# Kernel optimization log

Measured on AMD Instinct MI355X. Metric: run time of the kernel, lower is better.

The kernel has to match this reference:

```python
import jax, jax.numpy as jnp
import numpy as np

BS, T, NN, NF = 4, 64, 128, 16
HID, HEADS, RH, LD = 64, 4, 256, 64
EPG = 1024  # edges per graph


def _gat(x, src, dst, N, W, a_s, a_d, b, heads, out_dim, concat):
    # x: [N, Fin] -> h: [N, H, F]
    h = (x @ W).reshape(N, heads, out_dim)
    al_s = jnp.sum(h * a_s[None], axis=-1)  # [N, H]
    al_d = jnp.sum(h * a_d[None], axis=-1)
    e = jax.nn.leaky_relu(al_s[src] + al_d[dst], 0.2)  # [E, H]
    m = jax.ops.segment_max(e, dst, num_segments=N)
    m = jnp.where(jnp.isfinite(m), m, 0.0)
    ex = jnp.exp(e - m[dst])
    den = jax.ops.segment_sum(ex, dst, num_segments=N)
    alpha = ex / (den[dst] + 1e-16)
    agg = jax.ops.segment_sum(h[src] * alpha[:, :, None], dst, num_segments=N)
    o = agg.reshape(N, heads * out_dim) if concat else agg.mean(axis=1)
    return o + b


def _lstm(xs, Wih, Whh, bih, bhh, H):
    # xs: [T, B, D]; PyTorch gate order i,f,g,o
    B = xs.shape[1]
    h0 = jnp.zeros((B, H), xs.dtype)
    c0 = jnp.zeros((B, H), xs.dtype)

    def step(carry, xt):
        h, c = carry
        g = xt @ Wih.T + h @ Whh.T + bih + bhh
        i, f, gg, o = jnp.split(g, 4, axis=-1)
        c = jax.nn.sigmoid(f) * c + jax.nn.sigmoid(i) * jnp.tanh(gg)
        h = jax.nn.sigmoid(o) * jnp.tanh(c)
        return (h, c), None

    (hT, _), _ = jax.lax.scan(step, (h0, c0), xs)
    return hT


def setup_inputs() -> dict:
    key = jax.random.key(0)
    ks = jax.random.split(key, 32)
    s = 0.1
    d = {
        'x': jax.random.normal(ks[0], (BS, T, NN, NF), jnp.float32),
        'edge_index': jax.random.randint(ks[1], (2, EPG), 0, NN),
        'gat0_W': s * jax.random.normal(ks[2], (NF, HEADS * HID)),
        'gat0_asrc': s * jax.random.normal(ks[3], (HEADS, HID)),
        'gat0_adst': s * jax.random.normal(ks[4], (HEADS, HID)),
        'gat0_b': jnp.zeros((HEADS * HID,)),
        'gat1_W': s * jax.random.normal(ks[5], (HEADS * HID, HEADS * HID)),
        'gat1_asrc': s * jax.random.normal(ks[6], (HEADS, HID)),
        'gat1_adst': s * jax.random.normal(ks[7], (HEADS, HID)),
        'gat1_b': jnp.zeros((HEADS * HID,)),
        'gat2_W': s * jax.random.normal(ks[8], (HEADS * HID, HID)),
        'gat2_asrc': s * jax.random.normal(ks[9], (1, HID)),
        'gat2_adst': s * jax.random.normal(ks[10], (1, HID)),
        'gat2_b': jnp.zeros((HID,)),
        'Wih_f': s * jax.random.normal(ks[11], (4 * RH, HID)),
        'Whh_f': s * jax.random.normal(ks[12], (4 * RH, RH)),
        'bih_f': jnp.zeros((4 * RH,)),
        'bhh_f': jnp.zeros((4 * RH,)),
        'Wih_b': s * jax.random.normal(ks[13], (4 * RH, HID)),
        'Whh_b': s * jax.random.normal(ks[14], (4 * RH, RH)),
        'bih_b': jnp.zeros((4 * RH,)),
        'bhh_b': jnp.zeros((4 * RH,)),
        'mu_W': s * jax.random.normal(ks[15], (LD, 2 * RH)),
        'mu_b': jnp.zeros((LD,)),
        'lv_W': s * jax.random.normal(ks[16], (LD, 2 * RH)),
        'lv_b': jnp.zeros((LD,)),
    }
    return d


def reference(x, edge_index, gat0_W, gat0_asrc, gat0_adst, gat0_b,
              gat1_W, gat1_asrc, gat1_adst, gat1_b,
              gat2_W, gat2_asrc, gat2_adst, gat2_b,
              Wih_f, Whh_f, bih_f, bhh_f, Wih_b, Whh_b, bih_b, bhh_b,
              mu_W, mu_b, lv_W, lv_b):
    bs, t, nn, nf = x.shape
    ng = bs * t
    N = ng * nn
    xt = x.reshape(N, nf)
    # batch the edge index: repeat per graph with node offset, then add self-loops
    off = (jnp.arange(ng) * nn).repeat(edge_index.shape[1])  # [ng*E]
    bsrc = jnp.tile(edge_index[0], ng) + off
    bdst = jnp.tile(edge_index[1], ng) + off
    loops = jnp.arange(N)
    src = jnp.concatenate([bsrc, loops])
    dst = jnp.concatenate([bdst, loops])

    xt = jax.nn.relu(_gat(xt, src, dst, N, gat0_W, gat0_asrc, gat0_adst, gat0_b, HEADS, HID, True))
    xt = jax.nn.relu(_gat(xt, src, dst, N, gat1_W, gat1_asrc, gat1_adst, gat1_b, HEADS, HID, True))
    xt = jax.nn.relu(_gat(xt, src, dst, N, gat2_W, gat2_asrc, gat2_adst, gat2_b, 1, HID, False))

    batch_idx = jnp.arange(ng).repeat(nn)
    graph_embs = jax.ops.segment_sum(xt, batch_idx, num_segments=ng).reshape(bs, t, HID)

    seq = jnp.transpose(graph_embs, (1, 0, 2))  # [T, B, HID]
    h_fwd = _lstm(seq, Wih_f, Whh_f, bih_f, bhh_f, RH)
    h_bwd = _lstm(seq[::-1], Wih_b, Whh_b, bih_b, bhh_b, RH)
    feat = jnp.concatenate([h_fwd, h_bwd], axis=1)  # [B, 2*RH]

    mu = feat @ mu_W.T + mu_b
    logvar = feat @ lv_W.T + lv_b
    # PoincareBall(c=1).projx, float32 eps = 4e-3
    maxnorm = 1.0 - 4e-3
    nrm = jnp.linalg.norm(mu, axis=-1, keepdims=True)
    mu = jnp.where(nrm > maxnorm, mu / nrm * maxnorm, mu)
    return (mu, logvar)
```

## Files before the change

kernel.cpp:

```cpp
#include <hip/hip_runtime.h>
#include <hip/hip_bf16.h>

#define BSZ 4
#define TT 64
#define NNODE 128
#define NFEAT 16
#define HIDD 64
#define NHEAD 4
#define RHID 256
#define LDIM 64
#define EPG 1024
#define NGRAPH (BSZ*TT)
#define NTOT (NGRAPH*NNODE)
#define ESLOTS (EPG+NNODE)

#define WOFF_G0W 0
#define WOFF_G0AS 4096
#define WOFF_G0AD 4352
#define WOFF_G0B 4608
#define WOFF_G1W 4864
#define WOFF_G1AS 70400
#define WOFF_G1AD 70656
#define WOFF_G1B 70912
#define WOFF_G2W 71168
#define WOFF_G2AS 87552
#define WOFF_G2AD 87616
#define WOFF_G2B 87680
#define WOFF_WIHF 87744
#define WOFF_WHHF 153280
#define WOFF_BIHF 415424
#define WOFF_BHHF 416448
#define WOFF_WIHB 417472
#define WOFF_WHHB 483008
#define WOFF_BIHB 745152
#define WOFF_BHHB 746176
#define WOFF_MUW 747200
#define WOFF_MUB 779968
#define WOFF_LVW 780032
#define WOFF_LVB 812800
#define WTOTAL   812864

#define FOFF_WBUF 4096
#define FOFF_CSR  1052672
#define FOFF_SYNC 1314816
#define FOFF_WE   1576960
#define FOFF_BBF  1900000
#define FOFF_XFP  2756608
#define FOFF_XBP  3018752
#define FOFF_HT   3280896
#define FOFF_XSEQ 3282944
#define FOFF_PA   3291136
#define FOFF_PB   5388288
#define FOFF_P    7485440

#define BOFF_G0 0
#define BOFF_G1 4096
#define BOFF_G2 69632
#define BOFF_WF 86016
#define BOFF_WB 151552
#define BTOTAL  217088

#define SP_CVTX  (WTOTAL + BTOTAL)
#define SP_WHH   (SP_CVTX + NTOT*NFEAT)
#define SP_HX    (SP_WHH + 262144)
#define SP_TOTAL (SP_HX + 12288)

#define SENT 0xFFFFFFFFu

typedef __attribute__((ext_vector_type(8))) short short8;
typedef __attribute__((ext_vector_type(4))) float float4v;

__device__ __forceinline__ float b2f(unsigned short u){
  union { unsigned int i; float f; } v; v.i = ((unsigned int)u) << 16; return v.f;
}
__device__ __forceinline__ unsigned short f2b(float f){
  __hip_bfloat16 h = __float2bfloat16(f);
  union { __hip_bfloat16 h; unsigned short u; } v; v.h = h; return v.u;
}
__device__ __forceinline__ float ldf(const void* p, int i, int flag){
  return flag ? b2f(((const unsigned short*)p)[i]) : ((const float*)p)[i];
}
__device__ __forceinline__ float h2f(unsigned short s){
  union { _Float16 hh; unsigned short s; } u; u.s = s; return (float)u.hh;
}
__device__ __forceinline__ unsigned short f2h(float f){
  union { _Float16 hh; unsigned short s; } u; u.hh = (_Float16)f; return u.s;
}
__device__ __forceinline__ int sniff32(const unsigned short* w){
  int ok = 0;
  #pragma unroll
  for (int i = 0; i < 32; ++i){
    float a = fabsf(b2f(w[2 * i]));
    if (a > 1e-8f && a < 4.f) ok++;
  }
  return ok >= 16 ? 1 : 0;
}

struct CvtArgs {
  const void* src[24];
  int off[25];
};
__global__ void setup_kernel(CvtArgs a,
                             float* __restrict__ W, unsigned short* __restrict__ BBF,
                             unsigned short* __restrict__ P, unsigned int* __restrict__ WT,
                             unsigned int* __restrict__ HX,
                             const void* __restrict__ x, const int* __restrict__ ei,
                             int* __restrict__ csr_row, unsigned short* __restrict__ csr_src)
{
  __shared__ int cnt[NNODE];
  __shared__ int off[NNODE];
  __shared__ int wo[NNODE];
  const int tid = threadIdx.x;

  if (blockIdx.x == gridDim.x - 1){
    if (tid < NNODE) cnt[tid] = 0;
    __syncthreads();
    for (int i = tid; i < ESLOTS; i += 256){
      int d = (i < EPG) ? ei[EPG + i] : (i - EPG);
      atomicAdd(&cnt[d], 1);
    }
    __syncthreads();
    if (tid < NNODE) off[tid] = cnt[tid];
    for (int o = 1; o < NNODE; o <<= 1){
      __syncthreads();
      int t = (tid < NNODE && tid >= o) ? off[tid - o] : 0;
      __syncthreads();
      if (tid < NNODE) off[tid] += t;
    }
    __syncthreads();
    if (tid < NNODE){
      wo[tid] = off[tid] - cnt[tid];
      csr_row[tid + 1] = off[tid];
    }
    if (tid == 0) csr_row[0] = 0;
    __syncthreads();
    for (int i = tid; i < ESLOTS; i += 256){
      int s, d;
      if (i < EPG){ s = ei[i]; d = ei[EPG + i]; } else { s = i - EPG; d = i - EPG; }
      int pos = atomicAdd(&wo[d], 1);
      csr_src[pos] = (unsigned short)s;
    }
    return;
  }

  int id = blockIdx.x * blockDim.x + tid;
  if (id >= SP_TOTAL) return;
  int fl = sniff32((const unsigned short*)a.src[0]);
  if (id < WTOTAL){
    int k = 0;
    while (id >= a.off[k + 1]) ++k;
    W[id] = ldf(a.src[k], id - a.off[k], fl);
  } else if (id < WTOTAL + BTOTAL){
    int r = id - WTOTAL;
    float v;
    if (r < BOFF_G1){
      int o = r >> 4, k = r & 15;
      v = ldf(a.src[0], k * 256 + o, fl);
    } else if (r < BOFF_G2){
      int rr = r - BOFF_G1; int o = rr >> 8, k = rr & 255;
      v = ldf(a.src[4], k * 256 + o, fl);
    } else if (r < BOFF_WF){
      int rr = r - BOFF_G2; int o = rr >> 8, k = rr & 255;
      v = ldf(a.src[8], k * 64 + o, fl);
    } else if (r < BOFF_WB){
      int q = r - BOFF_WF; int k = q >> 10, n = q & 1023;
      v = ldf(a.src[12], n * 64 + k, fl);
    } else {
      int q = r - BOFF_WB; int k = q >> 10, n = q & 1023;
      v = ldf(a.src[16], n * 64 + k, fl);
    }
    BBF[r] = f2b(v);
  } else if (id < SP_CVTX + NTOT * NFEAT){
    int r = id - SP_CVTX;
    P[r] = fl ? ((const unsigned short*)x)[r] : f2b(((const float*)x)[r]);
  } else if (id < SP_HX){
    int r0 = id - SP_WHH;
    int c = r0 & 3;
    int lane = (r0 >> 2) & 63;
    int nt = (r0 >> 8) & 15;
    int kc = (r0 >> 12) & 7;
    int m = (r0 >> 15) & 3;
    int dir = r0 >> 17;
    int l = nt * 16 + (lane & 15);
    int u = (l >> 6) * 256 + 64 * m + (l & 63);
    int k0 = kc * 32 + ((lane >> 4) << 3) + 2 * c;
    const void* Wsrc = dir ? a.src[17] : a.src[13];
    unsigned short va = f2b(ldf(Wsrc, u * RHID + k0, fl));
    unsigned short vb = f2b(ldf(Wsrc, u * RHID + k0 + 1, fl));
    WT[r0] = (unsigned int)va | ((unsigned int)vb << 16);
  } else {
    HX[id - SP_HX] = SENT;
  }
}

template<int KV>
__global__ __launch_bounds__(256)
void glayer_kernel(const unsigned short* __restrict__ Pin,
                   const unsigned short* __restrict__ BT,
                   const float* __restrict__ Wbuf,
                   int asoff, int adoff, int boff,
                   const int* __restrict__ csr_row, const unsigned short* __restrict__ csr_src,
                   unsigned short* __restrict__ Pout)
{
  __shared__ unsigned short HT_[128 * 136];
  __shared__ unsigned short AD[128 * 136];
  __shared__ unsigned short ALS16[256];
  __shared__ unsigned short ALD16[256];
  __shared__ int   rowL[132];
  __shared__ unsigned char srcL[1152];

  const int tid = threadIdx.x;
  const int g = blockIdx.x >> 1, hb = blockIdx.x & 1;
  const int c0 = hb * 128;
  const int w = tid >> 6, lane = tid & 63, q = lane >> 4, r = lane & 15;
  unsigned short* Bst = AD;

  for (int i = tid; i < 129; i += 256) rowL[i] = csr_row[i];
  for (int i = tid; i < 1152; i += 256) srcL[i] = (unsigned char)csr_src[i];
  __syncthreads();

  {
    float4v acc0[8], acc1[8];
    #pragma unroll
    for (int i = 0; i < 8; ++i){ acc0[i] = (float4v){0,0,0,0}; acc1[i] = (float4v){0,0,0,0}; }
    const int KR = (KV + 31) / 32;
    for (int kr = 0; kr < KR; ++kr){
      const int kc = kr * 32;
      __syncthreads();
      {
        int n = tid >> 1, kb = (tid & 1) * 16;
        uint4 z = {0,0,0,0}; uint4 v0 = z, v1 = z;
        if (kb < KV)     v0 = *(const uint4*)(BT + (size_t)(c0 + n) * KV + kc + kb);
        if (kb + 8 < KV) v1 = *(const uint4*)(BT + (size_t)(c0 + n) * KV + kc + kb + 8);
        *(uint4*)&Bst[n * 40 + kb] = v0;
        *(uint4*)&Bst[n * 40 + kb + 8] = v1;
      }
      short8 a0 = {0,0,0,0,0,0,0,0}, a1 = {0,0,0,0,0,0,0,0};
      if (KV >= 32 || q < 2){
        a0 = *(const short8*)(Pin + (size_t)(g * 128 + 16 * w       + r) * KV + kc + q * 8);
        a1 = *(const short8*)(Pin + (size_t)(g * 128 + 16 * (w + 4) + r) * KV + kc + q * 8);
      }
      __syncthreads();
      #pragma unroll
      for (int nt = 0; nt < 8; ++nt){
        short8 bf = *(const short8*)&Bst[(16 * nt + r) * 40 + q * 8];
        acc0[nt] = __builtin_amdgcn_mfma_f32_16x16x32_bf16(a0, bf, acc0[nt], 0, 0, 0);
        acc1[nt] = __builtin_amdgcn_mfma_f32_16x16x32_bf16(a1, bf, acc1[nt], 0, 0, 0);
      }
    }
    __syncthreads();
    #pragma unroll
    for (int nt = 0; nt < 8; ++nt)
      #pragma unroll
      for (int i = 0; i < 4; ++i){
        HT_[(16 * nt + r) * 136 + 16 * w       + q * 4 + i] = f2b(acc0[nt][i]);
        HT_[(16 * nt + r) * 136 + 16 * (w + 4) + q * 4 + i] = f2b(acc1[nt][i]);
      }
    __syncthreads();
  }

  {
    float as0 = Wbuf[asoff + c0 + 2 * lane], as1 = Wbuf[asoff + c0 + 2 * lane + 1];
    float ad0 = Wbuf[adoff + c0 + 2 * lane], ad1 = Wbuf[adoff + c0 + 2 * lane + 1];
    for (int it = 0; it < 32; ++it){
      int n = it * 4 + w;
      float e0 = b2f(HT_[(2 * lane) * 136 + n]);
      float e1 = b2f(HT_[(2 * lane + 1) * 136 + n]);
      float vs = e0 * as0 + e1 * as1;
      float vd = e0 * ad0 + e1 * ad1;
      #pragma unroll
      for (int m = 16; m >= 1; m >>= 1){ vs += __shfl_xor(vs, m); vd += __shfl_xor(vd, m); }
      if ((lane & 31) == 0){
        ALS16[n * 2 + (lane >> 5)] = f2h(vs);
        ALD16[n * 2 + (lane >> 5)] = f2h(vd);
      }
    }
  }
  __syncthreads();

  for (int hl = 0; hl < 2; ++hl){
    for (int i = tid; i < 8704; i += 256) ((unsigned int*)AD)[i] = 0;
    __syncthreads();
    if (tid < 128){
      int n = tid;
      float aldv = h2f(ALD16[n * 2 + hl]);
      int rs = rowL[n], re = rowL[n + 1];
      float mx = -3e38f, den = 0.f;
      for (int j = rs; j < re; ++j){
        float v = h2f(ALS16[srcL[j] * 2 + hl]) + aldv;
        v = v > 0.f ? v : 0.2f * v;
        if (v > mx){ den = den * __expf(mx - v) + 1.f; mx = v; }
        else den += __expf(v - mx);
      }
      float iden = 1.f / (den + 1e-16f);
      for (int j = rs; j < re; ++j){
        float v = h2f(ALS16[srcL[j] * 2 + hl]) + aldv;
        v = v > 0.f ? v : 0.2f * v;
        float al = __expf(v - mx) * iden;
        int s = srcL[j];
        AD[n * 136 + s] = f2b(b2f(AD[n * 136 + s]) + al);
      }
    }
    __syncthreads();
    float4v am[2][4];
    #pragma unroll
    for (int mt = 0; mt < 2; ++mt)
      #pragma unroll
      for (int nt = 0; nt < 4; ++nt) am[mt][nt] = (float4v){0,0,0,0};
    #pragma unroll
    for (int kc = 0; kc < 4; ++kc){
      short8 af0 = *(const short8*)&AD[(w * 32      + r) * 136 + kc * 32 + q * 8];
      short8 af1 = *(const short8*)&AD[(w * 32 + 16 + r) * 136 + kc * 32 + q * 8];
      #pragma unroll
      for (int nt = 0; nt < 4; ++nt){
        short8 bf = *(const short8*)&HT_[(hl * 64 + nt * 16 + r) * 136 + kc * 32 + q * 8];
        am[0][nt] = __builtin_amdgcn_mfma_f32_16x16x32_bf16(af0, bf, am[0][nt], 0, 0, 0);
        am[1][nt] = __builtin_amdgcn_mfma_f32_16x16x32_bf16(af1, bf, am[1][nt], 0, 0, 0);
      }
    }
    #pragma unroll
    for (int mt = 0; mt < 2; ++mt)
      #pragma unroll
      for (int nt = 0; nt < 4; ++nt){
        int col = hl * 64 + nt * 16 + r;
        float bz = Wbuf[boff + c0 + col];
        #pragma unroll
        for (int i = 0; i < 4; ++i){
          int dst = w * 32 + mt * 16 + q * 4 + i;
          float v = am[mt][nt][i] + bz;
          v = v > 0.f ? v : 0.f;
          Pout[(size_t)(g * 128 + dst) * 256 + c0 + col] = f2b(v);
        }
      }
    __syncthreads();
  }
}

__global__ __launch_bounds__(256)
void glayer2_kernel(const unsigned short* __restrict__ Pin,
                    const unsigned short* __restrict__ BT,
                    const float* __restrict__ Wbuf,
                    const int* __restrict__ csr_row, const unsigned short* __restrict__ csr_src,
                    unsigned short* __restrict__ XSEQ)
{
  __shared__ unsigned short HT_[64 * 136];
  __shared__ unsigned short AD[128 * 136];
  __shared__ float ALSf[128];
  __shared__ float ALDf[128];
  __shared__ int   rowL[132];
  __shared__ unsigned char srcL[1152];
  __shared__ float pools[4][64];

  const int tid = threadIdx.x;
  const int g = blockIdx.x >> 1, hb = blockIdx.x & 1;
  const int w = tid >> 6, lane = tid & 63, q = lane >> 4, r = lane & 15;
  unsigned short* Bst = AD;

  for (int i = tid; i < 129; i += 256) rowL[i] = csr_row[i];
  for (int i = tid; i < 1152; i += 256) srcL[i] = (unsigned char)csr_src[i];
  __syncthreads();

  {
    float4v acc0[4], acc1[4];
    #pragma unroll
    for (int i = 0; i < 4; ++i){ acc0[i] = (float4v){0,0,0,0}; acc1[i] = (float4v){0,0,0,0}; }
    for (int kr = 0; kr < 8; ++kr){
      const int kc = kr * 32;
      __syncthreads();
      {
        int n = tid >> 2, kb = (tid & 3) * 8;
        uint4 v = *(const uint4*)(BT + (size_t)n * 256 + kc + kb);
        *(uint4*)&Bst[n * 40 + kb] = v;
      }
      short8 a0 = *(const short8*)(Pin + (size_t)(g * 128 + 16 * w       + r) * 256 + kc + q * 8);
      short8 a1 = *(const short8*)(Pin + (size_t)(g * 128 + 16 * (w + 4) + r) * 256 + kc + q * 8);
      __syncthreads();
      #pragma unroll
      for (int nt = 0; nt < 4; ++nt){
        short8 bf = *(const short8*)&Bst[(16 * nt + r) * 40 + q * 8];
        acc0[nt] = __builtin_amdgcn_mfma_f32_16x16x32_bf16(a0, bf, acc0[nt], 0, 0, 0);
        acc1[nt] = __builtin_amdgcn_mfma_f32_16x16x32_bf16(a1, bf, acc1[nt], 0, 0, 0);
      }
    }
    __syncthreads();
    #pragma unroll
    for (int nt = 0; nt < 4; ++nt)
      #pragma unroll
      for (int i = 0; i < 4; ++i){
        HT_[(16 * nt + r) * 136 + 16 * w       + q * 4 + i] = f2b(acc0[nt][i]);
        HT_[(16 * nt + r) * 136 + 16 * (w + 4) + q * 4 + i] = f2b(acc1[nt][i]);
      }
    __syncthreads();
  }

  {
    float asv = Wbuf[WOFF_G2AS + lane];
    float adv = Wbuf[WOFF_G2AD + lane];
    for (int it = 0; it < 32; ++it){
      int n = it * 4 + w;
      float e0 = b2f(HT_[lane * 136 + n]);
      float vs = e0 * asv, vd = e0 * adv;
      #pragma unroll
      for (int m = 32; m >= 1; m >>= 1){ vs += __shfl_xor(vs, m); vd += __shfl_xor(vd, m); }
      if (lane == 0){ ALSf[n] = vs; ALDf[n] = vd; }
    }
  }
  __syncthreads();
  for (int i = tid; i < 8704; i += 256) ((unsigned int*)AD)[i] = 0;
  __syncthreads();
  if (tid < 128){
    int n = tid;
    float aldv = ALDf[n];
    int rs = rowL[n], re = rowL[n + 1];
    float mx = -3e38f, den = 0.f;
    for (int j = rs; j < re; ++j){
      float v = ALSf[srcL[j]] + aldv;
      v = v > 0.f ? v : 0.2f * v;
      if (v > mx){ den = den * __expf(mx - v) + 1.f; mx = v; }
      else den += __expf(v - mx);
    }
    float iden = 1.f / (den + 1e-16f);
    for (int j = rs; j < re; ++j){
      float v = ALSf[srcL[j]] + aldv;
      v = v > 0.f ? v : 0.2f * v;
      float al = __expf(v - mx) * iden;
      int s = srcL[j];
      AD[n * 136 + s] = f2b(b2f(AD[n * 136 + s]) + al);
    }
  }
  __syncthreads();
  float4v am[2][4];
  #pragma unroll
  for (int mt = 0; mt < 2; ++mt)
    #pragma unroll
    for (int nt = 0; nt < 4; ++nt) am[mt][nt] = (float4v){0,0,0,0};
  #pragma unroll
  for (int kc = 0; kc < 4; ++kc){
    short8 af0 = *(const short8*)&AD[(w * 32      + r) * 136 + kc * 32 + q * 8];
    short8 af1 = *(const short8*)&AD[(w * 32 + 16 + r) * 136 + kc * 32 + q * 8];
    #pragma unroll
    for (int nt = 0; nt < 4; ++nt){
      short8 bf = *(const short8*)&HT_[(nt * 16 + r) * 136 + kc * 32 + q * 8];
      am[0][nt] = __builtin_amdgcn_mfma_f32_16x16x32_bf16(af0, bf, am[0][nt], 0, 0, 0);
      am[1][nt] = __builtin_amdgcn_mfma_f32_16x16x32_bf16(af1, bf, am[1][nt], 0, 0, 0);
    }
  }
  float psum[4] = {0.f, 0.f, 0.f, 0.f};
  #pragma unroll
  for (int nt = 0; nt < 4; ++nt){
    int col = nt * 16 + r;
    float bz = Wbuf[WOFF_G2B + col];
    #pragma unroll
    for (int mt = 0; mt < 2; ++mt)
      #pragma unroll
      for (int i = 0; i < 4; ++i){
        float v = am[mt][nt][i] + bz;
        psum[nt] += (v > 0.f ? v : 0.f);
      }
    psum[nt] += __shfl_xor(psum[nt], 16);
    psum[nt] += __shfl_xor(psum[nt], 32);
  }
  if (q == 0){
    #pragma unroll
    for (int nt = 0; nt < 4; ++nt) pools[w][nt * 16 + r] = psum[nt];
  }
  __syncthreads();
  if (tid < 64 && (tid >> 5) == hb){
    float s = pools[0][tid] + pools[1][tid] + pools[2][tid] + pools[3][tid];
    int b = g >> 6, tq = g & 63;
    XSEQ[(size_t)(tq * BSZ + b) * HIDD + tid] = f2b(s);
  }
}

__global__ __launch_bounds__(256)
void mmx2_kernel(const unsigned short* __restrict__ A,
                 const unsigned short* __restrict__ B0, const unsigned short* __restrict__ B1,
                 float* __restrict__ C0, float* __restrict__ C1, int M, int Nc, int K)
{
  __shared__ unsigned short As[64][40];
  __shared__ unsigned short Bs[64][40];
  const unsigned short* Bb = blockIdx.z ? B1 : B0;
  float* C = blockIdx.z ? C1 : C0;
  const int tid = threadIdx.x;
  const int w = tid >> 6, lane = tid & 63, q = lane >> 4, r = lane & 15;
  const int m0 = blockIdx.x * 64, n0 = blockIdx.y * 64;
  float4v acc0 = {0,0,0,0}, acc1 = {0,0,0,0}, acc2 = {0,0,0,0}, acc3 = {0,0,0,0};
  const int arow = tid >> 2, akb = (tid & 3) * 8;
  const int bk = tid >> 3, bnb = (tid & 7) * 8;
  for (int kc = 0; kc < K; kc += 32){
    int kw = K - kc; if (kw > 32) kw = 32;
    if (akb < kw){
      uint4 v = *(const uint4*)(A + (size_t)(m0 + arow) * K + kc + akb);
      *(uint4*)&As[arow][akb] = v;
    } else {
      uint4 z = {0,0,0,0}; *(uint4*)&As[arow][akb] = z;
    }
    if (bk < kw){
      uint4 v = *(const uint4*)(Bb + (size_t)(kc + bk) * Nc + n0 + bnb);
      const unsigned short* vs = (const unsigned short*)&v;
      #pragma unroll
      for (int e = 0; e < 8; ++e) Bs[bnb + e][bk] = vs[e];
    } else {
      #pragma unroll
      for (int e = 0; e < 8; ++e) Bs[bnb + e][bk] = 0;
    }
    __syncthreads();
    short8 af = *(const short8*)&As[16 * w + r][q * 8];
    short8 b0 = *(const short8*)&Bs[r][q * 8];
    short8 b1 = *(const short8*)&Bs[16 + r][q * 8];
    short8 b2 = *(const short8*)&Bs[32 + r][q * 8];
    short8 b3 = *(const short8*)&Bs[48 + r][q * 8];
    acc0 = __builtin_amdgcn_mfma_f32_16x16x32_bf16(af, b0, acc0, 0, 0, 0);
    acc1 = __builtin_amdgcn_mfma_f32_16x16x32_bf16(af, b1, acc1, 0, 0, 0);
    acc2 = __builtin_amdgcn_mfma_f32_16x16x32_bf16(af, b2, acc2, 0, 0, 0);
    acc3 = __builtin_amdgcn_mfma_f32_16x16x32_bf16(af, b3, acc3, 0, 0, 0);
    __syncthreads();
  }
  const int row = m0 + 16 * w + q * 4, col0 = n0 + r;
  #pragma unroll
  for (int i = 0; i < 4; ++i){
    size_t base = (size_t)(row + i) * Nc;
    C[base + col0]      = acc0[i];
    C[base + col0 + 16] = acc1[i];
    C[base + col0 + 32] = acc2[i];
    C[base + col0 + 48] = acc3[i];
  }
}

__global__ __launch_bounds__(256)
void lstm13_kernel(const float* __restrict__ XF, const float* __restrict__ XB,
                   const unsigned int* __restrict__ WT,
                   const float* __restrict__ bih_f, const float* __restrict__ bhh_f,
                   const float* __restrict__ bih_b, const float* __restrict__ bhh_b,
                   unsigned int* __restrict__ HX,
                   float* __restrict__ HT)
{
  __shared__ unsigned int WL[32768];
  __shared__ unsigned int H16[16 * 132];
  __shared__ float glds[4][256];

  const int tid = threadIdx.x;
  const int m = blockIdx.x & 3, dir = blockIdx.x >> 2;
  const int w = tid >> 6, lane = tid & 63, quad = lane >> 4, r = lane & 15;
  const float* Xp = dir ? XB : XF;
  const int ub = tid >> 6, uj = tid & 63;
  unsigned int* HXd = HX + dir * 6144;

  const float* bi = dir ? bih_b : bih_f;
  const float* bh = dir ? bhh_b : bhh_f;
  float bias0 = bi[0 * 256 + 64 * m + uj] + bh[0 * 256 + 64 * m + uj];
  float bias1 = bi[1 * 256 + 64 * m + uj] + bh[1 * 256 + 64 * m + uj];
  float bias2 = bi[2 * 256 + 64 * m + uj] + bh[2 * 256 + 64 * m + uj];
  float bias3 = bi[3 * 256 + 64 * m + uj] + bh[3 * 256 + 64 * m + uj];

  {
    const uint4* WT4 = (const uint4*)(WT + dir * 131072 + m * 32768);
    uint4* WL4 = (uint4*)WL;
    #pragma unroll
    for (int s = 0; s < 32; ++s)
      WL4[s * 256 + tid] = WT4[s * 256 + tid];
  }
  for (int i = tid; i < 16 * 132; i += 256) H16[i] = 0;
  float c = 0.f;
  __syncthreads();

  const uint4* WL4 = (const uint4*)WL;
  const uint4* H16u4 = (const uint4*)H16;

  float4v acc[4];
  auto kchunk = [&](int kc){
    uint4 av = H16u4[(lane & 15) * 33 + kc * 4 + quad];
    short8 af = *(const short8*)&av;
    #pragma unroll
    for (int t = 0; t < 4; ++t){
      int nt = w * 4 + t;
      uint4 bv = WL4[(kc * 16 + nt) * 64 + lane];
      short8 bf = *(const short8*)&bv;
      acc[t] = __builtin_amdgcn_mfma_f32_16x16x32_bf16(af, bf, acc[t], 0, 0, 0);
    }
  };

  for (int t = 0; t < TT; ++t){
    const int tb = dir ? (TT - 1 - t) : t;
    const float* xr = Xp + (size_t)(tb * 4 + ub) * 1024 + 64 * m + uj;
    float x0 = xr[0], x1 = xr[256], x2 = xr[512], x3 = xr[768];

    #pragma unroll
    for (int i = 0; i < 4; ++i) acc[i] = (float4v){0,0,0,0};
    kchunk(2 * m); kchunk(2 * m + 1);
    if (t > 0 && w > 0){
      int qp = (m + w) & 3;
      unsigned int* S = HXd + ((t - 1) % 3) * 2048 + m * 512;
      int b2 = lane >> 5, p2 = lane & 31;
      int i1G = b2 * 128 + 32 * qp + p2;
      int i2G = (b2 + 2) * 128 + 32 * qp + p2;
      int i1L = b2 * 132 + 32 * qp + p2;
      int i2L = (b2 + 2) * 132 + 32 * qp + p2;
      unsigned int v1, v2;
      int guard = 0;
      while ((v1 = __hip_atomic_load(&S[i1G], __ATOMIC_RELAXED, __HIP_MEMORY_SCOPE_AGENT)) == SENT
             && guard < 200000){ __builtin_amdgcn_s_sleep(1); ++guard; }
      guard = 0;
      while ((v2 = __hip_atomic_load(&S[i2G], __ATOMIC_RELAXED, __HIP_MEMORY_SCOPE_AGENT)) == SENT
             && guard < 200000){ __builtin_amdgcn_s_sleep(1); ++guard; }
      H16[i1L] = v1; H16[i2L] = v2;
      __hip_atomic_store(&S[i1G], SENT, __ATOMIC_RELAXED, __HIP_MEMORY_SCOPE_AGENT);
      __hip_atomic_store(&S[i2G], SENT, __ATOMIC_RELAXED, __HIP_MEMORY_SCOPE_AGENT);
    }
    __syncthreads();
    #pragma unroll
    for (int i = 1; i < 4; ++i){
      int qp = (m + i) & 3;
      kchunk(2 * qp); kchunk(2 * qp + 1);
    }
    if (quad == 0){
      #pragma unroll
      for (int tt = 0; tt < 4; ++tt){
        int l = (w * 4 + tt) * 16 + r;
        glds[0][l] = acc[tt][0];
        glds[1][l] = acc[tt][1];
        glds[2][l] = acc[tt][2];
        glds[3][l] = acc[tt][3];
      }
    }
    __syncthreads();

    float gi = glds[ub][uj]        + bias0 + x0;
    float gf = glds[ub][64 + uj]   + bias1 + x1;
    float gg = glds[ub][128 + uj]  + bias2 + x2;
    float go = glds[ub][192 + uj]  + bias3 + x3;
    float si = 1.f / (1.f + __expf(-gi));
    float sf = 1.f / (1.f + __expf(-gf));
    float so = 1.f / (1.f + __expf(-go));
    float tg = 1.f - 2.f / (1.f + __expf(2.f * gg));
    c = sf * c + si * tg;
    float ch = 1.f - 2.f / (1.f + __expf(2.f * c));
    float hval = so * ch;
    if (t == TT - 1){
      HT[(size_t)(dir * 4 + ub) * RHID + (64 * m + uj)] = hval;
      break;
    }
    unsigned int own = f2b(hval);
    unsigned int partner = ((unsigned int)__shfl_xor((int)own, 1)) & 0xffffu;
    unsigned int* S = HXd + (t % 3) * 2048;
    if ((uj & 1) == 0){
      unsigned int v = own | (partner << 16);
      int p = uj >> 1;
      int idxG = ub * 128 + 32 * m + p;
      int idxL = ub * 132 + 32 * m + p;
      H16[idxL] = v;
      #pragma unroll
      for (int cns = 1; cns < 4; ++cns)
        __hip_atomic_store(&S[((m + cns) & 3) * 512 + idxG], v,
                           __ATOMIC_RELAXED, __HIP_MEMORY_SCOPE_AGENT);
    }
    __syncthreads();
  }
}

__global__ __launch_bounds__(512)
void head2_kernel(const float* __restrict__ HT,
                  const float* __restrict__ muW, const float* __restrict__ mub,
                  const float* __restrict__ lvW, const float* __restrict__ lvb,
                  float* __restrict__ out)
{
  __shared__ float feat[4][512];
  __shared__ float muv[4][64];
  __shared__ float lvv[4][64];
  int tid = threadIdx.x;
  for (int i = tid; i < 2048; i += 512){
    int rr = i >> 8, k = i & 255;
    int b = rr & 3, d = rr >> 2;
    feat[b][d * 256 + k] = HT[i];
  }
  __syncthreads();
  int w = tid >> 6, lane = tid & 63;
  for (int job = w; job < 512; job += 8){
    int j = job & 63, b = (job >> 6) & 3, mat = job >> 8;
    const float* W = (mat ? lvW : muW) + (size_t)j * 512;
    float s = 0.f;
    #pragma unroll
    for (int e = 0; e < 8; ++e) s += W[lane * 8 + e] * feat[b][lane * 8 + e];
    #pragma unroll
    for (int mm = 32; mm >= 1; mm >>= 1) s += __shfl_xor(s, mm);
    if (lane == 0){
      float v = s + (mat ? lvb[j] : mub[j]);
      if (mat) lvv[b][j] = v; else muv[b][j] = v;
    }
  }
  __syncthreads();
  if (tid < 256){
    int b = tid >> 6, j = tid & 63;
    float mu = muv[b][j];
    float sq = mu * mu;
    #pragma unroll
    for (int mm = 32; mm >= 1; mm >>= 1) sq += __shfl_xor(sq, mm);
    float nrm = sqrtf(sq);
    const float mxn = 1.0f - 4e-3f;
    if (nrm > mxn) mu = mu / nrm * mxn;
    out[b * 64 + j] = mu;
    out[256 + b * 64 + j] = lvv[b][j];
  }
}

extern "C" void kernel_launch(void* const* d_in, const int* in_sizes, int n_in,
                              void* d_out, int out_size, void* d_ws, size_t ws_size,
                              hipStream_t stream)
{
  const int* ei = (const int*)d_in[1];

  float* FW   = (float*)d_ws;
  float* Wbuf = FW + FOFF_WBUF;
  int*   csr_row = (int*)(FW + FOFF_CSR);
  unsigned short* csr_src = (unsigned short*)(FW + FOFF_CSR + 132);
  float* XFp  = FW + FOFF_XFP;
  float* XBp  = FW + FOFF_XBP;
  float* HT   = FW + FOFF_HT;
  unsigned short* XSEQ = (unsigned short*)(FW + FOFF_XSEQ);
  unsigned short* PA   = (unsigned short*)(FW + FOFF_PA);
  unsigned short* PB   = (unsigned short*)(FW + FOFF_PB);
  unsigned short* Pb   = (unsigned short*)(FW + FOFF_P);
  unsigned int*   WT   = (unsigned int*)(FW + FOFF_WE);
  unsigned short* BBF  = (unsigned short*)(FW + FOFF_BBF);
  unsigned int*   HX   = (unsigned int*)(FW + FOFF_SYNC);

  CvtArgs ca;
  static const int wsz[24] = {4096,256,256,256, 65536,256,256,256, 16384,64,64,64,
                              65536,262144,1024,1024, 65536,262144,1024,1024,
                              32768,64,32768,64};
  {
    int acc = 0;
    for (int k = 0; k < 24; ++k){ ca.src[k] = d_in[2 + k]; ca.off[k] = acc; acc += wsz[k]; }
    ca.off[24] = acc;
  }
  int nblk = (SP_TOTAL + 255) / 256 + 1;
  setup_kernel<<<nblk, 256, 0, stream>>>(ca, Wbuf, BBF, Pb, WT, HX,
                                         d_in[0], ei, csr_row, csr_src);

  glayer_kernel<16><<<512, 256, 0, stream>>>(Pb, BBF + BOFF_G0, Wbuf,
                                             WOFF_G0AS, WOFF_G0AD, WOFF_G0B,
                                             csr_row, csr_src, PA);
  glayer_kernel<256><<<512, 256, 0, stream>>>(PA, BBF + BOFF_G1, Wbuf,
                                              WOFF_G1AS, WOFF_G1AD, WOFF_G1B,
                                              csr_row, csr_src, PB);
  glayer2_kernel<<<512, 256, 0, stream>>>(PB, BBF + BOFF_G2, Wbuf,
                                          csr_row, csr_src, XSEQ);

  mmx2_kernel<<<dim3(4, 16, 2), 256, 0, stream>>>(XSEQ, BBF + BOFF_WF, BBF + BOFF_WB,
                                                  XFp, XBp, 256, 1024, 64);

  lstm13_kernel<<<8, 256, 0, stream>>>(XFp, XBp, WT,
                                       Wbuf + WOFF_BIHF, Wbuf + WOFF_BHHF,
                                       Wbuf + WOFF_BIHB, Wbuf + WOFF_BHHB,
                                       HX, HT);

  head2_kernel<<<1, 512, 0, stream>>>(HT, Wbuf + WOFF_MUW, Wbuf + WOFF_MUB,
                                      Wbuf + WOFF_LVW, Wbuf + WOFF_LVB, (float*)d_out);
}
```

Baseline: 360.2 us.

## Fuse output head into LSTM kernel via atomic completion counter

Removes the separate head kernel launch by having all 8 LSTM blocks increment a global done counter, with block 0 waiting on it and then computing the mu/logvar projections and Poincare projection. The counter is zeroed in the setup kernel's HX region. The local-chunk MFMA that previously ran before the H exchange sync now runs after the barrier with the others, which removes that overlap. The trailing per-step __syncthreads is dropped. This saves one launch but adds a spin-wait and a serial head computation on 4 waves, and the dropped barrier may risk an H16 race between steps.

```diff
diff --git a/kernel.cpp b/kernel.cpp
--- a/kernel.cpp
+++ b/kernel.cpp
@@ -63,7 +63,7 @@
 #define SP_CVTX  (WTOTAL + BTOTAL)
 #define SP_WHH   (SP_CVTX + NTOT*NFEAT)
 #define SP_HX    (SP_WHH + 262144)
-#define SP_TOTAL (SP_HX + 12288)
+#define SP_TOTAL (SP_HX + 12288 + 64)
 
 #define SENT 0xFFFFFFFFu
 
@@ -189,7 +189,8 @@
     unsigned short vb = f2b(ldf(Wsrc, u * RHID + k0 + 1, fl));
     WT[r0] = (unsigned int)va | ((unsigned int)vb << 16);
   } else {
-    HX[id - SP_HX] = SENT;
+    int r0 = id - SP_HX;
+    HX[r0] = (r0 < 12288) ? SENT : 0u;
   }
 }
 
@@ -528,16 +529,18 @@
 }
 
 __global__ __launch_bounds__(256)
-void lstm13_kernel(const float* __restrict__ XF, const float* __restrict__ XB,
+void lstm14_kernel(const float* __restrict__ XF, const float* __restrict__ XB,
                    const unsigned int* __restrict__ WT,
-                   const float* __restrict__ bih_f, const float* __restrict__ bhh_f,
-                   const float* __restrict__ bih_b, const float* __restrict__ bhh_b,
+                   const float* __restrict__ Wbuf,
                    unsigned int* __restrict__ HX,
-                   float* __restrict__ HT)
+                   float* __restrict__ HT,
+                   float* __restrict__ out)
 {
   __shared__ unsigned int WL[32768];
   __shared__ unsigned int H16[16 * 132];
   __shared__ float glds[4][256];
+  __shared__ float muv[4][64];
+  __shared__ float lvv[4][64];
 
   const int tid = threadIdx.x;
   const int m = blockIdx.x & 3, dir = blockIdx.x >> 2;
@@ -545,9 +548,10 @@
   const float* Xp = dir ? XB : XF;
   const int ub = tid >> 6, uj = tid & 63;
   unsigned int* HXd = HX + dir * 6144;
-
-  const float* bi = dir ? bih_b : bih_f;
-  const float* bh = dir ? bhh_b : bhh_f;
+  int* DONE = (int*)(HX + 12288);
+
+  const float* bi = Wbuf + (dir ? WOFF_BIHB : WOFF_BIHF);
+  const float* bh = Wbuf + (dir ? WOFF_BHHB : WOFF_BHHF);
   float bias0 = bi[0 * 256 + 64 * m + uj] + bh[0 * 256 + 64 * m + uj];
   float bias1 = bi[1 * 256 + 64 * m + uj] + bh[1 * 256 + 64 * m + uj];
   float bias2 = bi[2 * 256 + 64 * m + uj] + bh[2 * 256 + 64 * m + uj];
@@ -587,7 +591,7 @@
 
     #pragma unroll
     for (int i = 0; i < 4; ++i) acc[i] = (float4v){0,0,0,0};
-    kchunk(2 * m); kchunk(2 * m + 1);
+
     if (t > 0 && w > 0){
       int qp = (m + w) & 3;
       unsigned int* S = HXd + ((t - 1) % 3) * 2048 + m * 512;
@@ -608,8 +612,9 @@
       __hip_atomic_store(&S[i2G], SENT, __ATOMIC_RELAXED, __HIP_MEMORY_SCOPE_AGENT);
     }
     __syncthreads();
-    #pragma unroll
-    for (int i = 1; i < 4; ++i){
+
+    #pragma unroll
+    for (int i = 0; i < 4; ++i){
       int qp = (m + i) & 3;
       kchunk(2 * qp); kchunk(2 * qp + 1);
     }
@@ -654,42 +659,37 @@
         __hip_atomic_store(&S[((m + cns) & 3) * 512 + idxG], v,
                            __ATOMIC_RELAXED, __HIP_MEMORY_SCOPE_AGENT);
     }
-    __syncthreads();
-  }
-}
-
-__global__ __launch_bounds__(512)
-void head2_kernel(const float* __restrict__ HT,
-                  const float* __restrict__ muW, const float* __restrict__ mub,
-                  const float* __restrict__ lvW, const float* __restrict__ lvb,
-                  float* __restrict__ out)
-{
-  __shared__ float feat[4][512];
-  __shared__ float muv[4][64];
-  __shared__ float lvv[4][64];
-  int tid = threadIdx.x;
-  for (int i = tid; i < 2048; i += 512){
-    int rr = i >> 8, k = i & 255;
-    int b = rr & 3, d = rr >> 2;
-    feat[b][d * 256 + k] = HT[i];
-  }
-  __syncthreads();
-  int w = tid >> 6, lane = tid & 63;
-  for (int job = w; job < 512; job += 8){
+  }
+
+  __syncthreads();
+  if (tid == 0)
+    __hip_atomic_fetch_add(DONE, 1, __ATOMIC_RELEASE, __HIP_MEMORY_SCOPE_AGENT);
+  if (blockIdx.x != 0) return;
+  if (tid == 0){
+    int guard = 0;
+    while (__hip_atomic_load(DONE, __ATOMIC_ACQUIRE, __HIP_MEMORY_SCOPE_AGENT) < 8
+           && guard < 2000000){ __builtin_amdgcn_s_sleep(1); ++guard; }
+  }
+  __syncthreads();
+  for (int job = w; job < 512; job += 4){
     int j = job & 63, b = (job >> 6) & 3, mat = job >> 8;
-    const float* W = (mat ? lvW : muW) + (size_t)j * 512;
+    const float* W = Wbuf + (mat ? WOFF_LVW : WOFF_MUW) + (size_t)j * 512;
     float s = 0.f;
     #pragma unroll
-    for (int e = 0; e < 8; ++e) s += W[lane * 8 + e] * feat[b][lane * 8 + e];
+    for (int e = 0; e < 8; ++e){
+      int dk = lane * 8 + e;
+      float fv = HT[((dk >> 8) * 4 + b) * 256 + (dk & 255)];
+      s += W[dk] * fv;
+    }
     #pragma unroll
     for (int mm = 32; mm >= 1; mm >>= 1) s += __shfl_xor(s, mm);
     if (lane == 0){
-      float v = s + (mat ? lvb[j] : mub[j]);
+      float v = s + Wbuf[(mat ? WOFF_LVB : WOFF_MUB) + j];
       if (mat) lvv[b][j] = v; else muv[b][j] = v;
     }
   }
   __syncthreads();
-  if (tid < 256){
+  {
     int b = tid >> 6, j = tid & 63;
     float mu = muv[b][j];
     float sq = mu * mu;
@@ -749,11 +749,5 @@
   mmx2_kernel<<<dim3(4, 16, 2), 256, 0, stream>>>(XSEQ, BBF + BOFF_WF, BBF + BOFF_WB,
                                                   XFp, XBp, 256, 1024, 64);
 
-  lstm13_kernel<<<8, 256, 0, stream>>>(XFp, XBp, WT,
-                                       Wbuf + WOFF_BIHF, Wbuf + WOFF_BHHF,
-                                       Wbuf + WOFF_BIHB, Wbuf + WOFF_BHHB,
-                                       HX, HT);
-
-  head2_kernel<<<1, 512, 0, stream>>>(HT, Wbuf + WOFF_MUW, Wbuf + WOFF_MUB,
-                                      Wbuf + WOFF_LVW, Wbuf + WOFF_LVB, (float*)d_out);
-}
+  lstm14_kernel<<<8, 256, 0, stream>>>(XFp, XBp, WT, Wbuf, HX, HT, (float*)d_out);
+}
```

Result: slower. 458.3 us (+27.3%).
